# Optimization experiments

Measured on AMD Instinct MI355X. Metric: run time of the kernel, lower is better.

The kernel has to match this reference:

```python
import jax, jax.numpy as jnp
import numpy as np

BLOCK = 128          # fp8 quantization block size (from linear_deepseek_v3)
FP8_MAX = 448.0      # max representable value of float8_e4m3fn
F8 = jnp.float8_e4m3fn
G, T, K, N = 8, 1024, 7168, 2048


def setup_inputs() -> dict:
    key = jax.random.key(0)
    kx, kw, kb = jax.random.split(key, 3)
    xs = jax.random.normal(kx, (G, T, K), jnp.float32)
    # Build an fp8 block-quantized weight + per-(128x128)-block fp32 scale,
    # matching the stored self.weight (fp8) and self.scale parameters.
    w_raw = jax.random.normal(kw, (G, N, K), jnp.float32)
    wb = w_raw.reshape(G, N // BLOCK, BLOCK, K // BLOCK, BLOCK)
    amax = jnp.max(jnp.abs(wb), axis=(2, 4))            # [G, NB, KB]
    scale = amax / FP8_MAX
    w_q = (wb / scale[:, :, None, :, None]).astype(F8).astype(jnp.float32)
    weight = w_q.reshape(G, N, K)                        # fp8 code values held in fp32
    bias = jax.random.normal(kb, (G, N), jnp.float32) * 0.02
    return {"xs": xs, "weight": weight, "scale": scale, "bias": bias}


def reference(xs, weight, scale, bias):
    """Grouped fp8 block-quantized GEMM with inline dequant.
    xs:     [G, T, K] fp32 activations (one slab per group)
    weight: [G, N, K] fp8-quantized weights (stored as fp32 code values)
    scale:  [G, N/128, K/128] fp32 per-block weight scales
    bias:   [G, N] fp32
    """
    g, t, k = xs.shape
    n = weight.shape[1]
    kb, nb = k // BLOCK, n // BLOCK
    # --- act_quant_deepseek_v3: per (token, 128-col block) absmax/448 scale ---
    xb = xs.reshape(g, t, kb, BLOCK)
    a_scale = jnp.max(jnp.abs(xb), axis=-1) / FP8_MAX        # [G, T, KB]
    x_q = (xb / a_scale[..., None]).astype(F8).astype(jnp.float32)
    x_deq = (x_q * a_scale[..., None]).reshape(g, t, k)      # fused dequant
    # --- weight dequant: broadcast per-(128x128)-block scale ---
    w_deq = (weight.reshape(g, nb, BLOCK, kb, BLOCK)
             * scale[:, :, None, :, None]).reshape(g, n, k)
    # --- grouped GEMM (y = x A^T) + bias, fp32 accumulation ---
    y = jnp.einsum('gtk,gnk->gtn', x_deq, w_deq) + bias[:, None, :]
    return y
```

## Files before the change

kernel.cpp:

```cpp
#include <hip/hip_runtime.h>
#include <hip/hip_bf16.h>
#include <stdint.h>

#define G_ 8
#define T_ 1024
#define K_ 7168
#define N_ 2048
#define KB_ 56
#define NB_ 16
#define NT8_ 56

#define ACT_WGS  57344
#define WREC_WGS 28672

typedef __attribute__((ext_vector_type(4))) float f32x4;
typedef __attribute__((ext_vector_type(8))) int   i32x8;

typedef __attribute__((address_space(3))) uint32_t lds_u32_t;
typedef const __attribute__((address_space(1))) uint32_t gbl_u32_t;

__device__ __forceinline__ void gload_lds16(const void* gsrc, const void* ldst)
{
    __builtin_amdgcn_global_load_lds(
        (gbl_u32_t*)(uintptr_t)gsrc,
        (lds_u32_t*)(uint32_t)(uintptr_t)ldst, 16, 0, 0);
}

__device__ __forceinline__ void blockbar()
{
    asm volatile("" ::: "memory");
    __builtin_amdgcn_s_barrier();
    asm volatile("" ::: "memory");
}

__global__ __launch_bounds__(256) void prep_kernel(
    const float* __restrict__ xs, uint8_t* __restrict__ xq8,
    float* __restrict__ ascale,
    const float* __restrict__ w, uint8_t* __restrict__ wq8)
{
    const int bid = blockIdx.x;
    if (bid < ACT_WGS) {
        const int grp = (bid * 256 + threadIdx.x) >> 5;
        const int l   = threadIdx.x & 31;
        const size_t base = (size_t)grp * 128 + (size_t)l * 4;

        const float4 v = *(const float4*)(xs + base);
        float am = fmaxf(fmaxf(fabsf(v.x), fabsf(v.y)),
                         fmaxf(fabsf(v.z), fabsf(v.w)));
#pragma unroll
        for (int off = 1; off <= 16; off <<= 1)
            am = fmaxf(am, __shfl_xor(am, off, 64));

        const float rs = 448.0f / am;
        const float s  = am * (1.0f / 448.0f);

        int pk = __builtin_amdgcn_cvt_pk_fp8_f32(v.x * rs, v.y * rs, 0, false);
        pk     = __builtin_amdgcn_cvt_pk_fp8_f32(v.z * rs, v.w * rs, pk, true);
        *(uint32_t*)(xq8 + base) = (uint32_t)pk;

        if (l == 0) {
            const int kb = grp % KB_;
            const int t  = (grp / KB_) & (T_ - 1);
            const int g  = grp / (KB_ * T_);
            ascale[(((size_t)(g * 4 + (t >> 8))) * KB_ + kb) * 256 + (t & 255)] = s;
        }
    } else {
        const size_t i = ((size_t)(bid - ACT_WGS) * 256 + threadIdx.x) * 16;
        uint32_t o[4];
#pragma unroll
        for (int q = 0; q < 4; ++q) {
            const float4 a = *(const float4*)(w + i + q * 4);
            int pk = __builtin_amdgcn_cvt_pk_fp8_f32(a.x, a.y, 0, false);
            pk     = __builtin_amdgcn_cvt_pk_fp8_f32(a.z, a.w, pk, true);
            o[q] = (uint32_t)pk;
        }
        *(uint4*)(wq8 + i) = make_uint4(o[0], o[1], o[2], o[3]);
    }
}

union Frag { i32x8 v; struct { int4 lo, hi; } p; };

#define RD_FRAG(dst, base, r)                                                 \
  { const int rx_ = ((r) & 7) << 4;                                           \
    const char* bp_ = smem + (base) + (r)*128;                                \
    dst.p.lo = *(const int4*)(bp_ + ((lhi*32) ^ rx_));                        \
    dst.p.hi = *(const int4*)(bp_ + ((lhi*32 + 16) ^ rx_)); }

#define STG_A(c, t, bb) gload_lds16(pA8[c] + (size_t)(t)*128,                 \
      smem + (bb)*16384 + (c)*4096 + tid*16)
#define STG_B(c, t, bb) gload_lds16(pB8[c] + (size_t)(t)*128,                 \
      smem + 32768 + (bb)*16384 + (c)*4096 + tid*16)
#define STG_S(c) gload_lds16(pS + (size_t)(c)*2048,                           \
      smem + 65536 + ((c)&1)*4096 + tid*16)

__global__ __launch_bounds__(256, 2) void gemm_fp8_kernel(
    const uint8_t* __restrict__ xq8, const uint8_t* __restrict__ wq8,
    const float* __restrict__ ascale, const float* __restrict__ wscale,
    const float* __restrict__ bias, float* __restrict__ y)
{
    __shared__ char smem[73952];

    const int bx0 = blockIdx.x;
    const int g     = bx0 & 7;
    const int inner = bx0 >> 3;
    const int tn    = inner & 15;
    const int tm    = inner >> 4;
    const int t0 = tm * 128, n0 = tn * 128;

    const int tid = threadIdx.x, lane = tid & 63, wid = tid >> 6;
    const int l15 = lane & 15, lhi = lane >> 4;
    const int wrow = (wid >> 1) * 64;
    const int wcol = (wid & 1) * 64;

    const uint8_t* Ag = xq8 + (size_t)g * T_ * K_;
    const uint8_t* Bg = wq8 + (size_t)g * N_ * K_;

    const int srow = tid >> 3;
    const int xoff = ((tid & 7) ^ (srow & 7)) * 16;
    const uint8_t* pA8[4];
    const uint8_t* pB8[4];
#pragma unroll
    for (int c = 0; c < 4; ++c) {
        pA8[c] = Ag + (size_t)(t0 + c * 32 + srow) * K_ + xoff;
        pB8[c] = Bg + (size_t)(n0 + c * 32 + srow) * K_ + xoff;
    }

    const float* pS = ascale + ((size_t)(g * 4 + (tm >> 1)) * KB_) * 256
                    + (tid >> 5) * 256 + (tm & 1) * 128 + (tid & 31) * 4;

    const f32x4 z4 = {0.f, 0.f, 0.f, 0.f};
    f32x4 acc[4][4] = {};
    Frag bF[4];

    if (tid < KB_) {
        const float wv = wscale[((size_t)(g * NB_ + tn)) * KB_ + tid];
        *(float*)(smem + 73728 + tid * 4) = wv;
    }
    STG_S(0);
#pragma unroll
    for (int c = 0; c < 4; ++c) { STG_A(c, 0, 0); STG_B(c, 0, 0); }
    asm volatile("s_waitcnt vmcnt(0)" ::: "memory");
    asm volatile("s_waitcnt lgkmcnt(0)" ::: "memory");
    blockbar();

    for (int u = 0; u < NT8_; ++u) {
        const int cur = u & 1, nxt = cur ^ 1;
        const bool pf = (u + 1 < NT8_);
        const int sbuf = (u >> 3) & 1;

        if ((u & 7) == 0 && u + 8 < NT8_) STG_S((u >> 3) + 1);
        if (pf) {
#pragma unroll
            for (int c = 0; c < 4; ++c) { STG_A(c, u + 1, nxt); STG_B(c, u + 1, nxt); }
        }

        const float wsc = *(const float*)(smem + 73728 + u * 4);

#pragma unroll
        for (int n = 0; n < 4; ++n)
            RD_FRAG(bF[n], 32768 + cur * 16384, wcol + n * 16 + l15);

        __builtin_amdgcn_s_setprio(1);
#pragma unroll
        for (int m = 0; m < 4; ++m) {
            Frag aF;
            RD_FRAG(aF, cur * 16384, wrow + m * 16 + l15);
            const float4 sv = *(const float4*)(smem + 65536 + sbuf * 4096 +
                (u & 7) * 512 + (wrow + m * 16 + lhi * 4) * 4);
            const float a0 = sv.x * wsc, a1 = sv.y * wsc,
                        a2 = sv.z * wsc, a3 = sv.w * wsc;
#pragma unroll
            for (int n = 0; n < 4; ++n) {
                f32x4 blk = __builtin_amdgcn_mfma_scale_f32_16x16x128_f8f6f4(
                    aF.v, bF[n].v, z4, 0, 0, 0, 0x7F7F7F7F, 0, 0x7F7F7F7F);
                acc[m][n][0] += blk[0] * a0;
                acc[m][n][1] += blk[1] * a1;
                acc[m][n][2] += blk[2] * a2;
                acc[m][n][3] += blk[3] * a3;
            }
        }
        __builtin_amdgcn_s_setprio(0);

        if (pf) {
            asm volatile("s_waitcnt vmcnt(0)" ::: "memory");
            blockbar();
        }
    }

    float* Yg = y + (size_t)g * T_ * N_;
#pragma unroll
    for (int n = 0; n < 4; ++n) {
        const int col = n0 + wcol + n * 16 + l15;
        const float bv = bias[g * N_ + col];
#pragma unroll
        for (int m = 0; m < 4; ++m) {
            const int r0 = t0 + wrow + m * 16 + lhi * 4;
#pragma unroll
            for (int j = 0; j < 4; ++j)
                Yg[(size_t)(r0 + j) * N_ + col] = acc[m][n][j] + bv;
        }
    }
}

extern "C" void kernel_launch(void* const* d_in, const int* in_sizes, int n_in,
                              void* d_out, int out_size, void* d_ws, size_t ws_size,
                              hipStream_t stream)
{
    const float* xs     = (const float*)d_in[0];
    const float* weight = (const float*)d_in[1];
    const float* scale  = (const float*)d_in[2];
    const float* bias   = (const float*)d_in[3];
    float* y = (float*)d_out;

    uint8_t* xq8  = (uint8_t*)d_ws;
    float*   ascl = (float*)((char*)d_ws + 58720256);
    uint8_t* wq8  = (uint8_t*)((char*)d_ws + 60555264);

    prep_kernel<<<ACT_WGS + WREC_WGS, 256, 0, stream>>>(
        xs, xq8, ascl, weight, wq8);

    gemm_fp8_kernel<<<G_ * (T_ / 128) * (N_ / 128), 256, 0, stream>>>(
        xq8, wq8, ascl, scale, bias, y);
}
```

Baseline: 340.2 us.

## Fuse quantization prep and GEMM into one cooperative persistent kernel

Replaces the separate prep and GEMM launches with a single cooperative kernel of 512 workgroups. The workgroups grid-stride through activation and weight quantization, synchronize across the grid, and then each computes two GEMM tiles. This removes a kernel launch and the gap between the two phases. In exchange, the GEMM runs with only 512 persistent workgroups in two serial rounds, and the quantize phase loses the oversubscription it had before. The scale multiply is also hoisted and vectorized, and the old two-kernel path is kept as a fallback.

```diff
diff --git a/kernel.cpp b/kernel.cpp
--- a/kernel.cpp
+++ b/kernel.cpp
@@ -1,6 +1,9 @@
 #include <hip/hip_runtime.h>
 #include <hip/hip_bf16.h>
+#include <hip/hip_cooperative_groups.h>
 #include <stdint.h>
+
+namespace cg = cooperative_groups;
 
 #define G_ 8
 #define T_ 1024
@@ -12,6 +15,7 @@
 
 #define ACT_WGS  57344
 #define WREC_WGS 28672
+#define COOP_WGS 512
 
 typedef __attribute__((ext_vector_type(4))) float f32x4;
 typedef __attribute__((ext_vector_type(8))) int   i32x8;
@@ -33,49 +37,49 @@
     asm volatile("" ::: "memory");
 }
 
-__global__ __launch_bounds__(256) void prep_kernel(
-    const float* __restrict__ xs, uint8_t* __restrict__ xq8,
-    float* __restrict__ ascale,
-    const float* __restrict__ w, uint8_t* __restrict__ wq8)
-{
-    const int bid = blockIdx.x;
-    if (bid < ACT_WGS) {
-        const int grp = (bid * 256 + threadIdx.x) >> 5;
-        const int l   = threadIdx.x & 31;
-        const size_t base = (size_t)grp * 128 + (size_t)l * 4;
-
-        const float4 v = *(const float4*)(xs + base);
-        float am = fmaxf(fmaxf(fabsf(v.x), fabsf(v.y)),
-                         fmaxf(fabsf(v.z), fabsf(v.w)));
-#pragma unroll
-        for (int off = 1; off <= 16; off <<= 1)
-            am = fmaxf(am, __shfl_xor(am, off, 64));
-
-        const float rs = 448.0f / am;
-        const float s  = am * (1.0f / 448.0f);
-
-        int pk = __builtin_amdgcn_cvt_pk_fp8_f32(v.x * rs, v.y * rs, 0, false);
-        pk     = __builtin_amdgcn_cvt_pk_fp8_f32(v.z * rs, v.w * rs, pk, true);
-        *(uint32_t*)(xq8 + base) = (uint32_t)pk;
-
-        if (l == 0) {
-            const int kb = grp % KB_;
-            const int t  = (grp / KB_) & (T_ - 1);
-            const int g  = grp / (KB_ * T_);
-            ascale[(((size_t)(g * 4 + (t >> 8))) * KB_ + kb) * 256 + (t & 255)] = s;
-        }
-    } else {
-        const size_t i = ((size_t)(bid - ACT_WGS) * 256 + threadIdx.x) * 16;
-        uint32_t o[4];
-#pragma unroll
-        for (int q = 0; q < 4; ++q) {
-            const float4 a = *(const float4*)(w + i + q * 4);
-            int pk = __builtin_amdgcn_cvt_pk_fp8_f32(a.x, a.y, 0, false);
-            pk     = __builtin_amdgcn_cvt_pk_fp8_f32(a.z, a.w, pk, true);
-            o[q] = (uint32_t)pk;
-        }
-        *(uint4*)(wq8 + i) = make_uint4(o[0], o[1], o[2], o[3]);
-    }
+__device__ __forceinline__ void act_body(
+    int abid, int tid, const float* __restrict__ xs,
+    uint8_t* __restrict__ xq8, float* __restrict__ ascale)
+{
+    const int grp = (abid * 256 + tid) >> 5;
+    const int l   = tid & 31;
+    const size_t base = (size_t)grp * 128 + (size_t)l * 4;
+
+    const float4 v = *(const float4*)(xs + base);
+    float am = fmaxf(fmaxf(fabsf(v.x), fabsf(v.y)),
+                     fmaxf(fabsf(v.z), fabsf(v.w)));
+#pragma unroll
+    for (int off = 1; off <= 16; off <<= 1)
+        am = fmaxf(am, __shfl_xor(am, off, 64));
+
+    const float rs = 448.0f / am;
+    const float s  = am * (1.0f / 448.0f);
+
+    int pk = __builtin_amdgcn_cvt_pk_fp8_f32(v.x * rs, v.y * rs, 0, false);
+    pk     = __builtin_amdgcn_cvt_pk_fp8_f32(v.z * rs, v.w * rs, pk, true);
+    *(uint32_t*)(xq8 + base) = (uint32_t)pk;
+
+    if (l == 0) {
+        const int kb = grp % KB_;
+        const int t  = (grp / KB_) & (T_ - 1);
+        const int g  = grp / (KB_ * T_);
+        ascale[(((size_t)(g * 4 + (t >> 8))) * KB_ + kb) * 256 + (t & 255)] = s;
+    }
+}
+
+__device__ __forceinline__ void wrec_body(
+    int wbid, int tid, const float* __restrict__ w, uint8_t* __restrict__ wq8)
+{
+    const size_t i = ((size_t)wbid * 256 + tid) * 16;
+    uint32_t o[4];
+#pragma unroll
+    for (int q = 0; q < 4; ++q) {
+        const float4 a = *(const float4*)(w + i + q * 4);
+        int pk = __builtin_amdgcn_cvt_pk_fp8_f32(a.x, a.y, 0, false);
+        pk     = __builtin_amdgcn_cvt_pk_fp8_f32(a.z, a.w, pk, true);
+        o[q] = (uint32_t)pk;
+    }
+    *(uint4*)(wq8 + i) = make_uint4(o[0], o[1], o[2], o[3]);
 }
 
 union Frag { i32x8 v; struct { int4 lo, hi; } p; };
@@ -93,113 +97,156 @@
 #define STG_S(c) gload_lds16(pS + (size_t)(c)*2048,                           \
       smem + 65536 + ((c)&1)*4096 + tid*16)
 
+__device__ __forceinline__ void gemm_tile(
+    char* smem, int g, int inner, int tid,
+    const uint8_t* __restrict__ xq8, const uint8_t* __restrict__ wq8,
+    const float* __restrict__ ascale, const float* __restrict__ wscale,
+    const float* __restrict__ bias, float* __restrict__ y)
+{
+    const int tn = inner & 15;
+    const int tm = inner >> 4;
+    const int t0 = tm * 128, n0 = tn * 128;
+
+    const int lane = tid & 63, wid = tid >> 6;
+    const int l15 = lane & 15, lhi = lane >> 4;
+    const int wrow = (wid >> 1) * 64;
+    const int wcol = (wid & 1) * 64;
+
+    const uint8_t* Ag = xq8 + (size_t)g * T_ * K_;
+    const uint8_t* Bg = wq8 + (size_t)g * N_ * K_;
+
+    const int srow = tid >> 3;
+    const int xoff = ((tid & 7) ^ (srow & 7)) * 16;
+    const uint8_t* pA8[4];
+    const uint8_t* pB8[4];
+#pragma unroll
+    for (int c = 0; c < 4; ++c) {
+        pA8[c] = Ag + (size_t)(t0 + c * 32 + srow) * K_ + xoff;
+        pB8[c] = Bg + (size_t)(n0 + c * 32 + srow) * K_ + xoff;
+    }
+
+    const float* pS = ascale + ((size_t)(g * 4 + (tm >> 1)) * KB_) * 256
+                    + (tid >> 5) * 256 + (tm & 1) * 128 + (tid & 31) * 4;
+
+    const f32x4 z4 = {0.f, 0.f, 0.f, 0.f};
+    f32x4 acc[4][4] = {};
+    Frag bF[4];
+    f32x4 asv[4];
+
+    blockbar();
+    if (tid < KB_) {
+        const float wv = wscale[((size_t)(g * NB_ + tn)) * KB_ + tid];
+        *(float*)(smem + 73728 + tid * 4) = wv;
+    }
+    STG_S(0);
+#pragma unroll
+    for (int c = 0; c < 4; ++c) { STG_A(c, 0, 0); STG_B(c, 0, 0); }
+    asm volatile("s_waitcnt vmcnt(0)" ::: "memory");
+    asm volatile("s_waitcnt lgkmcnt(0)" ::: "memory");
+    blockbar();
+
+    for (int u = 0; u < NT8_; ++u) {
+        const int cur = u & 1, nxt = cur ^ 1;
+        const bool pf = (u + 1 < NT8_);
+        const int sbuf = (u >> 3) & 1;
+
+        if ((u & 7) == 0 && u + 8 < NT8_) STG_S((u >> 3) + 1);
+        if (pf) {
+#pragma unroll
+            for (int c = 0; c < 4; ++c) { STG_A(c, u + 1, nxt); STG_B(c, u + 1, nxt); }
+        }
+
+        const float wsc = *(const float*)(smem + 73728 + u * 4);
+
+#pragma unroll
+        for (int n = 0; n < 4; ++n)
+            RD_FRAG(bF[n], 32768 + cur * 16384, wcol + n * 16 + l15);
+#pragma unroll
+        for (int m = 0; m < 4; ++m) {
+            const float4 sv = *(const float4*)(smem + 65536 + sbuf * 4096 +
+                (u & 7) * 512 + (wrow + m * 16 + lhi * 4) * 4);
+            asv[m][0] = sv.x * wsc; asv[m][1] = sv.y * wsc;
+            asv[m][2] = sv.z * wsc; asv[m][3] = sv.w * wsc;
+        }
+
+        __builtin_amdgcn_s_setprio(1);
+#pragma unroll
+        for (int m = 0; m < 4; ++m) {
+            Frag aF;
+            RD_FRAG(aF, cur * 16384, wrow + m * 16 + l15);
+#pragma unroll
+            for (int n = 0; n < 4; ++n) {
+                f32x4 blk = __builtin_amdgcn_mfma_scale_f32_16x16x128_f8f6f4(
+                    aF.v, bF[n].v, z4, 0, 0, 0, 0x7F7F7F7F, 0, 0x7F7F7F7F);
+                acc[m][n] += blk * asv[m];
+            }
+        }
+        __builtin_amdgcn_s_setprio(0);
+
+        if (pf) {
+            asm volatile("s_waitcnt vmcnt(0)" ::: "memory");
+            blockbar();
+        }
+    }
+
+    float* Yg = y + (size_t)g * T_ * N_;
+#pragma unroll
+    for (int n = 0; n < 4; ++n) {
+        const int col = n0 + wcol + n * 16 + l15;
+        const float bv = bias[g * N_ + col];
+#pragma unroll
+        for (int m = 0; m < 4; ++m) {
+            const int r0 = t0 + wrow + m * 16 + lhi * 4;
+#pragma unroll
+            for (int j = 0; j < 4; ++j)
+                Yg[(size_t)(r0 + j) * N_ + col] = acc[m][n][j] + bv;
+        }
+    }
+}
+
+__global__ __launch_bounds__(256, 2) void fused_kernel(
+    const float* __restrict__ xs, const float* __restrict__ w,
+    const float* __restrict__ wscale, const float* __restrict__ bias,
+    uint8_t* __restrict__ xq8, float* __restrict__ ascale,
+    uint8_t* __restrict__ wq8, float* __restrict__ y)
+{
+    __shared__ char smem[73952];
+    const int b = blockIdx.x, tid = threadIdx.x;
+
+    for (int abid = b; abid < ACT_WGS; abid += COOP_WGS)
+        act_body(abid, tid, xs, xq8, ascale);
+    for (int wbid = b; wbid < WREC_WGS; wbid += COOP_WGS)
+        wrec_body(wbid, tid, w, wq8);
+
+    cg::this_grid().sync();
+
+    const int g = b & 7;
+#pragma unroll 1
+    for (int t = 0; t < 2; ++t) {
+        const int inner = (b >> 3) * 2 + t;
+        gemm_tile(smem, g, inner, tid, xq8, wq8, ascale, wscale, bias, y);
+    }
+}
+
+__global__ __launch_bounds__(256) void prep_kernel(
+    const float* __restrict__ xs, uint8_t* __restrict__ xq8,
+    float* __restrict__ ascale,
+    const float* __restrict__ w, uint8_t* __restrict__ wq8)
+{
+    const int bid = blockIdx.x;
+    if (bid < ACT_WGS) act_body(bid, threadIdx.x, xs, xq8, ascale);
+    else               wrec_body(bid - ACT_WGS, threadIdx.x, w, wq8);
+}
+
 __global__ __launch_bounds__(256, 2) void gemm_fp8_kernel(
     const uint8_t* __restrict__ xq8, const uint8_t* __restrict__ wq8,
     const float* __restrict__ ascale, const float* __restrict__ wscale,
     const float* __restrict__ bias, float* __restrict__ y)
 {
     __shared__ char smem[73952];
-
     const int bx0 = blockIdx.x;
-    const int g     = bx0 & 7;
-    const int inner = bx0 >> 3;
-    const int tn    = inner & 15;
-    const int tm    = inner >> 4;
-    const int t0 = tm * 128, n0 = tn * 128;
-
-    const int tid = threadIdx.x, lane = tid & 63, wid = tid >> 6;
-    const int l15 = lane & 15, lhi = lane >> 4;
-    const int wrow = (wid >> 1) * 64;
-    const int wcol = (wid & 1) * 64;
-
-    const uint8_t* Ag = xq8 + (size_t)g * T_ * K_;
-    const uint8_t* Bg = wq8 + (size_t)g * N_ * K_;
-
-    const int srow = tid >> 3;
-    const int xoff = ((tid & 7) ^ (srow & 7)) * 16;
-    const uint8_t* pA8[4];
-    const uint8_t* pB8[4];
-#pragma unroll
-    for (int c = 0; c < 4; ++c) {
-        pA8[c] = Ag + (size_t)(t0 + c * 32 + srow) * K_ + xoff;
-        pB8[c] = Bg + (size_t)(n0 + c * 32 + srow) * K_ + xoff;
-    }
-
-    const float* pS = ascale + ((size_t)(g * 4 + (tm >> 1)) * KB_) * 256
-                    + (tid >> 5) * 256 + (tm & 1) * 128 + (tid & 31) * 4;
-
-    const f32x4 z4 = {0.f, 0.f, 0.f, 0.f};
-    f32x4 acc[4][4] = {};
-    Frag bF[4];
-
-    if (tid < KB_) {
-        const float wv = wscale[((size_t)(g * NB_ + tn)) * KB_ + tid];
-        *(float*)(smem + 73728 + tid * 4) = wv;
-    }
-    STG_S(0);
-#pragma unroll
-    for (int c = 0; c < 4; ++c) { STG_A(c, 0, 0); STG_B(c, 0, 0); }
-    asm volatile("s_waitcnt vmcnt(0)" ::: "memory");
-    asm volatile("s_waitcnt lgkmcnt(0)" ::: "memory");
-    blockbar();
-
-    for (int u = 0; u < NT8_; ++u) {
-        const int cur = u & 1, nxt = cur ^ 1;
-        const bool pf = (u + 1 < NT8_);
-        const int sbuf = (u >> 3) & 1;
-
-        if ((u & 7) == 0 && u + 8 < NT8_) STG_S((u >> 3) + 1);
-        if (pf) {
-#pragma unroll
-            for (int c = 0; c < 4; ++c) { STG_A(c, u + 1, nxt); STG_B(c, u + 1, nxt); }
-        }
-
-        const float wsc = *(const float*)(smem + 73728 + u * 4);
-
-#pragma unroll
-        for (int n = 0; n < 4; ++n)
-            RD_FRAG(bF[n], 32768 + cur * 16384, wcol + n * 16 + l15);
-
-        __builtin_amdgcn_s_setprio(1);
-#pragma unroll
-        for (int m = 0; m < 4; ++m) {
-            Frag aF;
-            RD_FRAG(aF, cur * 16384, wrow + m * 16 + l15);
-            const float4 sv = *(const float4*)(smem + 65536 + sbuf * 4096 +
-                (u & 7) * 512 + (wrow + m * 16 + lhi * 4) * 4);
-            const float a0 = sv.x * wsc, a1 = sv.y * wsc,
-                        a2 = sv.z * wsc, a3 = sv.w * wsc;
-#pragma unroll
-            for (int n = 0; n < 4; ++n) {
-                f32x4 blk = __builtin_amdgcn_mfma_scale_f32_16x16x128_f8f6f4(
-                    aF.v, bF[n].v, z4, 0, 0, 0, 0x7F7F7F7F, 0, 0x7F7F7F7F);
-                acc[m][n][0] += blk[0] * a0;
-                acc[m][n][1] += blk[1] * a1;
-                acc[m][n][2] += blk[2] * a2;
-                acc[m][n][3] += blk[3] * a3;
-            }
-        }
-        __builtin_amdgcn_s_setprio(0);
-
-        if (pf) {
-            asm volatile("s_waitcnt vmcnt(0)" ::: "memory");
-            blockbar();
-        }
-    }
-
-    float* Yg = y + (size_t)g * T_ * N_;
-#pragma unroll
-    for (int n = 0; n < 4; ++n) {
-        const int col = n0 + wcol + n * 16 + l15;
-        const float bv = bias[g * N_ + col];
-#pragma unroll
-        for (int m = 0; m < 4; ++m) {
-            const int r0 = t0 + wrow + m * 16 + lhi * 4;
-#pragma unroll
-            for (int j = 0; j < 4; ++j)
-                Yg[(size_t)(r0 + j) * N_ + col] = acc[m][n][j] + bv;
-        }
-    }
+    gemm_tile(smem, bx0 & 7, bx0 >> 3, threadIdx.x,
+              xq8, wq8, ascale, wscale, bias, y);
 }
 
 extern "C" void kernel_launch(void* const* d_in, const int* in_sizes, int n_in,
@@ -216,9 +263,25 @@
     float*   ascl = (float*)((char*)d_ws + 58720256);
     uint8_t* wq8  = (uint8_t*)((char*)d_ws + 60555264);
 
-    prep_kernel<<<ACT_WGS + WREC_WGS, 256, 0, stream>>>(
-        xs, xq8, ascl, weight, wq8);
-
-    gemm_fp8_kernel<<<G_ * (T_ / 128) * (N_ / 128), 256, 0, stream>>>(
-        xq8, wq8, ascl, scale, bias, y);
-}
+    int dev = 0, coop = 0;
+    hipGetDevice(&dev);
+    hipDeviceGetAttribute(&coop, hipDeviceAttributeCooperativeLaunch, dev);
+
+    bool done = false;
+    if (coop) {
+        const float* a0 = xs;  const float* a1 = weight;
+        const float* a2 = scale; const float* a3 = bias;
+        uint8_t* a4 = xq8; float* a5 = ascl; uint8_t* a6 = wq8; float* a7 = y;
+        void* kargs[] = { &a0, &a1, &a2, &a3, &a4, &a5, &a6, &a7 };
+        hipError_t e = hipLaunchCooperativeKernel(
+            (const void*)fused_kernel, dim3(COOP_WGS), dim3(256),
+            kargs, 0, stream);
+        done = (e == hipSuccess);
+    }
+    if (!done) {
+        prep_kernel<<<ACT_WGS + WREC_WGS, 256, 0, stream>>>(
+            xs, xq8, ascl, weight, wq8);
+        gemm_fp8_kernel<<<G_ * (T_ / 128) * (N_ / 128), 256, 0, stream>>>(
+            xq8, wq8, ascl, scale, bias, y);
+    }
+}
```

New measurement: 422.7 us. 1.24x slower.
